# Performance work log

Measured on AMD Instinct MI355X. Metric: run time of the kernel, lower is better.

## Reference

```python
import jax, jax.numpy as jnp
import numpy as np

N = 50000      # nodes
E = 800000     # edges (before self loops)
IN_D = 128
HID = 128
OUT_D = 64
HEADS = 4
FH = HID // HEADS  # per-head feature dim
NEG_SLOPE = 0.2


def setup_inputs() -> dict:
    key = jax.random.key(0)
    ks = jax.random.split(key, 16)
    s = 0.05
    inp = {
        "x": jax.random.normal(ks[0], (N, IN_D), dtype=jnp.float32),
        "edge_index": jax.random.randint(ks[1], (2, E), 0, N, dtype=jnp.int32),
        "Wi": jax.random.normal(ks[2], (IN_D, HID), dtype=jnp.float32) * s,
        "bi": jnp.zeros((HID,), dtype=jnp.float32),
        "W0": jax.random.normal(ks[3], (HID, HID), dtype=jnp.float32) * s,
        "as0": jax.random.normal(ks[4], (HEADS, FH), dtype=jnp.float32) * s,
        "ad0": jax.random.normal(ks[5], (HEADS, FH), dtype=jnp.float32) * s,
        "b0": jnp.zeros((HID,), dtype=jnp.float32),
        "W1": jax.random.normal(ks[6], (HID, HID), dtype=jnp.float32) * s,
        "as1": jax.random.normal(ks[7], (HEADS, FH), dtype=jnp.float32) * s,
        "ad1": jax.random.normal(ks[8], (HEADS, FH), dtype=jnp.float32) * s,
        "b1": jnp.zeros((HID,), dtype=jnp.float32),
        "Wo": jax.random.normal(ks[9], (HID, OUT_D), dtype=jnp.float32) * s,
        "bo": jnp.zeros((OUT_D,), dtype=jnp.float32),
    }
    return inp


def _gat_layer(h, src, dst, W, a_src, a_dst, b):
    # h: [N, HID]; src/dst: [E'] (with self loops)
    hp = (h @ W).reshape(N, HEADS, FH)               # projected per-head features
    al_s = jnp.einsum('nhf,hf->nh', hp, a_src)       # [N, H]
    al_d = jnp.einsum('nhf,hf->nh', hp, a_dst)
    e = jax.nn.leaky_relu(al_s[src] + al_d[dst], NEG_SLOPE)  # [E', H]
    # neighbor softmax over incoming edges of each dst node (stable)
    m = jax.ops.segment_max(e, dst, num_segments=N)
    m = jnp.where(jnp.isfinite(m), m, 0.0)
    num = jnp.exp(e - m[dst])
    den = jax.ops.segment_sum(num, dst, num_segments=N)
    coef = num / (den[dst] + 1e-16)                  # [E', H]
    out = jax.ops.segment_sum(coef[:, :, None] * hp[src], dst, num_segments=N)
    return out.reshape(N, HID) + b


def reference(x, edge_index, Wi, bi, W0, as0, ad0, b0, W1, as1, ad1, b1, Wo, bo):
    # add self loops (PyG GATConv default)
    loop = jnp.arange(N, dtype=edge_index.dtype)
    src = jnp.concatenate([edge_index[0], loop])
    dst = jnp.concatenate([edge_index[1], loop])

    h = jax.nn.relu(x @ Wi + bi)
    # layer 0 (dropout = identity in eval)
    h = h + jax.nn.relu(_gat_layer(h, src, dst, W0, as0, ad0, b0))
    # layer 1
    h = h + jax.nn.relu(_gat_layer(h, src, dst, W1, as1, ad1, b1))
    return h @ Wo + bo
```

## Files before the change

### kernel.cpp

```cpp
#include <hip/hip_runtime.h>
#include <hip/hip_bf16.h>


__device__ __forceinline__ float lrelu(float x){ return x > 0.f ? x : 0.2f * x; }

typedef __attribute__((ext_vector_type(8))) short bf16x8;
typedef __attribute__((ext_vector_type(4))) float f32x4;

__device__ __forceinline__ ushort f2bf(float f){
    union { __hip_bfloat16 b; ushort u; } cv;
    cv.b = __float2bfloat16(f);
    return cv.u;
}
__device__ __forceinline__ float bf2f(short u){
    union { uint i; float f; } c;
    c.i = ((uint)(ushort)u) << 16;
    return c.f;
}

constexpr int CAP = 64;
constexpr int BUCKET_CAP = 8192;
constexpr int P1_EDGES = 2048;

__global__ __launch_bounds__(256) void bin_edges_kernel(
    const int* __restrict__ ei, int* __restrict__ gcur, int2* __restrict__ binned, int E, int N)
{
    __shared__ int hist[256], offs[256], gpos[256];
    __shared__ int2 stag[P1_EDGES];
    __shared__ int wsum[4];
    int tid = threadIdx.x;
    hist[tid] = 0;
    __syncthreads();

    int base = blockIdx.x * P1_EDGES;
    int srcv[8], dstv[8], rk[8];
    #pragma unroll
    for (int j = 0; j < 8; j++){
        int e = base + j * 256 + tid;
        if (e < E + N){
            int s, d;
            if (e < E){ s = ei[e]; d = ei[E + e]; } else { s = e - E; d = s; }
            srcv[j] = s; dstv[j] = d;
            rk[j] = atomicAdd(&hist[d >> 8], 1);
        } else dstv[j] = -1;
    }
    __syncthreads();

    int lane = tid & 63, wid = tid >> 6;
    int v = hist[tid];
    int x = v;
    #pragma unroll
    for (int o = 1; o < 64; o <<= 1){ int t = __shfl_up(x, o); if (lane >= o) x += t; }
    if (lane == 63) wsum[wid] = x;
    __syncthreads();
    int woff = 0;
    for (int w2 = 0; w2 < wid; w2++) woff += wsum[w2];
    offs[tid] = woff + x - v;
    __syncthreads();

    #pragma unroll
    for (int j = 0; j < 8; j++){
        if (dstv[j] >= 0){
            int b = dstv[j] >> 8;
            stag[offs[b] + rk[j]] = make_int2(srcv[j], dstv[j]);
        }
    }
    if (hist[tid] > 0) gpos[tid] = atomicAdd(&gcur[tid], hist[tid]);
    __syncthreads();

    int nE = offs[255] + hist[255];
    for (int i = tid; i < nE; i += 256){
        int2 p = stag[i];
        int b = p.y >> 8;
        int idx = gpos[b] + (i - offs[b]);
        if (idx < BUCKET_CAP) binned[(size_t)b * BUCKET_CAP + idx] = p;
    }
}

__global__ __launch_bounds__(256) void build_slots_kernel(
    const int* __restrict__ gcur, const int2* __restrict__ binned,
    int* __restrict__ cnt, int* __restrict__ slots, int N)
{
    __shared__ int cnt_l[256];
    __shared__ int slots_l[256][CAP];
    int tid = threadIdx.x;
    int b = blockIdx.x;
    cnt_l[tid] = 0;
    __syncthreads();

    int ne = gcur[b]; if (ne > BUCKET_CAP) ne = BUCKET_CAP;
    const int2* bp = binned + (size_t)b * BUCKET_CAP;
    for (int i = tid; i < ne; i += 256){
        int2 p = bp[i];
        int ld = p.y & 255;
        int pos = atomicAdd(&cnt_l[ld], 1);
        if (pos < CAP) slots_l[ld][pos] = p.x;
    }
    __syncthreads();

    int node = b * 256 + tid;
    if (node < N) cnt[node] = min(cnt_l[tid], CAP);
    for (int j = tid; j < 256 * CAP; j += 256){
        int n2 = b * 256 + (j >> 6);
        if (n2 < N) slots[(size_t)n2 * CAP + (j & 63)] = slots_l[j >> 6][j & 63];
    }
}

__global__ void wcast_all_kernel(const float* __restrict__ Wi, const float* __restrict__ W0,
                                 const float* __restrict__ W1, const float* __restrict__ Wo,
                                 ushort* __restrict__ ti, ushort* __restrict__ t0,
                                 ushort* __restrict__ t1, ushort* __restrict__ to_){
    int i = blockIdx.x * 256 + threadIdx.x;
    if (i < 16384){
        int k = i >> 7, n = i & 127;        ti[n * 128 + k] = f2bf(Wi[i]);
    } else if (i < 32768){
        int j = i - 16384; int k = j >> 7, n = j & 127;  t0[n * 128 + k] = f2bf(W0[j]);
    } else if (i < 49152){
        int j = i - 32768; int k = j >> 7, n = j & 127;  t1[n * 128 + k] = f2bf(W1[j]);
    } else if (i < 57344){
        int j = i - 49152; int k = j / 64, n = j % 64;   to_[n * 128 + k] = f2bf(Wo[j]);
    }
}

template<int NCOL, bool RELU, bool BIAS, bool BF16OUT, bool LOGITS, bool ABF16>
__global__ __launch_bounds__(256) void mfma_matmul_kernel(
    const void* __restrict__ Av,
    const ushort* __restrict__ Wt,
    const float* __restrict__ bias,
    void* __restrict__ Cv,
    const float* __restrict__ as_, const float* __restrict__ ad_,
    float* __restrict__ als, float* __restrict__ ald, int M)
{
    constexpr int NT = NCOL / 16;
    __shared__ ushort Ws[NCOL][136];
    int tid = threadIdx.x;
    for (int i = tid * 8; i < NCOL * 128; i += 256 * 8){
        int r = i >> 7, c = i & 127;
        *(uint4*)&Ws[r][c] = *(const uint4*)&Wt[i];
    }
    __syncthreads();

    int lane = tid & 63, wave = tid >> 6;
    int r15 = lane & 15;
    int ko  = (lane >> 4) * 8;
    int row  = blockIdx.x * 64 + wave * 16 + r15;
    int rowc = row < M ? row : M - 1;

    f32x4 acc[NT];
    #pragma unroll
    for (int t = 0; t < NT; t++) acc[t] = (f32x4){0.f, 0.f, 0.f, 0.f};

    #pragma unroll
    for (int kt = 0; kt < 4; ++kt){
        bf16x8 af;
        if (ABF16){
            af = *(const bf16x8*)&((const ushort*)Av)[(size_t)rowc * 128 + kt * 32 + ko];
        } else {
            const float* Arow = (const float*)Av + (size_t)rowc * 128;
            float4 a0 = *(const float4*)&Arow[kt * 32 + ko];
            float4 a1 = *(const float4*)&Arow[kt * 32 + ko + 4];
            af[0] = f2bf(a0.x); af[1] = f2bf(a0.y); af[2] = f2bf(a0.z); af[3] = f2bf(a0.w);
            af[4] = f2bf(a1.x); af[5] = f2bf(a1.y); af[6] = f2bf(a1.z); af[7] = f2bf(a1.w);
        }
        #pragma unroll
        for (int t = 0; t < NT; t++){
            bf16x8 bf = *(const bf16x8*)&Ws[t * 16 + r15][kt * 32 + ko];
            acc[t] = __builtin_amdgcn_mfma_f32_16x16x32_bf16(af, bf, acc[t], 0, 0, 0);
        }
    }

    int oc    = lane & 15;
    int orow0 = blockIdx.x * 64 + wave * 16 + (lane >> 4) * 4;
    #pragma unroll
    for (int t = 0; t < NT; t++){
        int ocol = t * 16 + oc;
        float bv = BIAS ? bias[ocol] : 0.f;
        #pragma unroll
        for (int rg = 0; rg < 4; rg++){
            int orow = orow0 + rg;
            if (orow < M){
                float v = acc[t][rg] + bv;
                if (RELU) v = fmaxf(v, 0.f);
                if (BF16OUT) ((ushort*)Cv)[(size_t)orow * NCOL + ocol] = f2bf(v);
                else         ((float*)Cv) [(size_t)orow * NCOL + ocol] = v;
            }
        }
    }

    if (LOGITS){
        float sva[4][4], svd[4][4];
        #pragma unroll
        for (int hh = 0; hh < 4; hh++){
            float as0v = as_[hh*32 + oc],      ad0v = ad_[hh*32 + oc];
            float as1v = as_[hh*32 + 16 + oc], ad1v = ad_[hh*32 + 16 + oc];
            #pragma unroll
            for (int rg = 0; rg < 4; rg++){
                sva[hh][rg] = acc[2*hh][rg] * as0v + acc[2*hh+1][rg] * as1v;
                svd[hh][rg] = acc[2*hh][rg] * ad0v + acc[2*hh+1][rg] * ad1v;
            }
        }
        #pragma unroll
        for (int o = 1; o < 16; o <<= 1){
            #pragma unroll
            for (int hh = 0; hh < 4; hh++)
                #pragma unroll
                for (int rg = 0; rg < 4; rg++){
                    sva[hh][rg] += __shfl_xor(sva[hh][rg], o);
                    svd[hh][rg] += __shfl_xor(svd[hh][rg], o);
                }
        }
        if (oc < 4){
            #pragma unroll
            for (int rg = 0; rg < 4; rg++){
                int orow = orow0 + rg;
                if (orow < M){
                    float va = (oc & 2) ? ((oc & 1) ? sva[3][rg] : sva[2][rg])
                                        : ((oc & 1) ? sva[1][rg] : sva[0][rg]);
                    float vd = (oc & 2) ? ((oc & 1) ? svd[3][rg] : svd[2][rg])
                                        : ((oc & 1) ? svd[1][rg] : svd[0][rg]);
                    als[orow * 4 + oc] = va;
                    ald[orow * 4 + oc] = vd;
                }
            }
        }
    }
}

__global__ __launch_bounds__(256) void gat_aggregate_kernel(
    const int* __restrict__ cnt, const int* __restrict__ slots,
    const ushort* __restrict__ hp, const float* __restrict__ als,
    const float* __restrict__ ald, const float* __restrict__ bias,
    ushort* __restrict__ h, int n)
{
    __shared__ float num_s[4][CAP * 5];
    __shared__ int   src_s[4][CAP];
    int wid = threadIdx.x >> 6;
    int lane = threadIdx.x & 63;
    int node = blockIdx.x * 4 + wid;
    float* nums = num_s[wid];
    int*   srcs = src_s[wid];

    int er = lane >> 4;
    int fg = (lane & 15) * 8;
    int head = (lane & 15) >> 2;
    int f2 = fg + er * 2;

    int deg = 0;
    float4 aldv = make_float4(0.f,0.f,0.f,0.f);
    float hold0 = 0.f, hold1 = 0.f;
    float bv0 = 0.f, bv1 = 0.f;
    if (node < n){
        deg = cnt[node];
        if (deg > CAP) deg = CAP;
        aldv = *(const float4*)&ald[node * 4];
        ushort2 h16 = *(const ushort2*)&h[(size_t)node * 128 + f2];
        hold0 = bf2f(h16.x); hold1 = bf2f(h16.y);
        bv0 = bias[f2]; bv1 = bias[f2 + 1];
    }

    float d0=0.f,d1=0.f,d2=0.f,d3=0.f;
    if (lane < deg){
        int s = slots[node * CAP + lane];
        srcs[lane] = s;
        float4 av = *(const float4*)&als[s * 4];
        d0 = __expf(lrelu(av.x + aldv.x));
        d1 = __expf(lrelu(av.y + aldv.y));
        d2 = __expf(lrelu(av.z + aldv.z));
        d3 = __expf(lrelu(av.w + aldv.w));
    }
    float s0=d0, s1=d1, s2=d2, s3=d3;
    #pragma unroll
    for (int o = 1; o < 64; o <<= 1){
        s0+=__shfl_xor(s0,o); s1+=__shfl_xor(s1,o);
        s2+=__shfl_xor(s2,o); s3+=__shfl_xor(s3,o);
    }
    float inv0=1.f/(s0+1e-16f), inv1=1.f/(s1+1e-16f);
    float inv2=1.f/(s2+1e-16f), inv3=1.f/(s3+1e-16f);
    if (lane < deg){
        nums[lane*5+0]=d0*inv0; nums[lane*5+1]=d1*inv1;
        nums[lane*5+2]=d2*inv2; nums[lane*5+3]=d3*inv3;
    }

    float a0=0.f,a1=0.f,a2=0.f,a3=0.f,a4=0.f,a5=0.f,a6=0.f,a7=0.f;
    for (int i = 0; i < deg; i += 8){
        int e0 = i + er, e1 = i + 4 + er;
        bool v0 = e0 < deg, v1 = e1 < deg;
        int ec0 = v0 ? e0 : 0, ec1 = v1 ? e1 : 0;
        int sA = srcs[ec0], sB = srcs[ec1];
        float c0 = nums[ec0*5 + head]; c0 = v0 ? c0 : 0.f;
        float c1 = nums[ec1*5 + head]; c1 = v1 ? c1 : 0.f;
        bf16x8 h0 = *(const bf16x8*)&hp[(size_t)sA * 128 + fg];
        bf16x8 h1 = *(const bf16x8*)&hp[(size_t)sB * 128 + fg];
        a0 = fmaf(c0, bf2f(h0[0]), a0); a1 = fmaf(c0, bf2f(h0[1]), a1);
        a2 = fmaf(c0, bf2f(h0[2]), a2); a3 = fmaf(c0, bf2f(h0[3]), a3);
        a4 = fmaf(c0, bf2f(h0[4]), a4); a5 = fmaf(c0, bf2f(h0[5]), a5);
        a6 = fmaf(c0, bf2f(h0[6]), a6); a7 = fmaf(c0, bf2f(h0[7]), a7);
        a0 = fmaf(c1, bf2f(h1[0]), a0); a1 = fmaf(c1, bf2f(h1[1]), a1);
        a2 = fmaf(c1, bf2f(h1[2]), a2); a3 = fmaf(c1, bf2f(h1[3]), a3);
        a4 = fmaf(c1, bf2f(h1[4]), a4); a5 = fmaf(c1, bf2f(h1[5]), a5);
        a6 = fmaf(c1, bf2f(h1[6]), a6); a7 = fmaf(c1, bf2f(h1[7]), a7);
    }
    a0 += __shfl_xor(a0,16); a0 += __shfl_xor(a0,32);
    a1 += __shfl_xor(a1,16); a1 += __shfl_xor(a1,32);
    a2 += __shfl_xor(a2,16); a2 += __shfl_xor(a2,32);
    a3 += __shfl_xor(a3,16); a3 += __shfl_xor(a3,32);
    a4 += __shfl_xor(a4,16); a4 += __shfl_xor(a4,32);
    a5 += __shfl_xor(a5,16); a5 += __shfl_xor(a5,32);
    a6 += __shfl_xor(a6,16); a6 += __shfl_xor(a6,32);
    a7 += __shfl_xor(a7,16); a7 += __shfl_xor(a7,32);

    if (node < n){
        float sA = (er & 2) ? ((er & 1) ? a6 : a4) : ((er & 1) ? a2 : a0);
        float sB = (er & 2) ? ((er & 1) ? a7 : a5) : ((er & 1) ? a3 : a1);
        float r0 = hold0 + fmaxf(sA + bv0, 0.f);
        float r1 = hold1 + fmaxf(sB + bv1, 0.f);
        ushort2 o2; o2.x = f2bf(r0); o2.y = f2bf(r1);
        *(ushort2*)&h[(size_t)node * 128 + f2] = o2;
    }
}

extern "C" void kernel_launch(void* const* d_in, const int* in_sizes, int n_in,
                              void* d_out, int out_size, void* d_ws, size_t ws_size,
                              hipStream_t stream)
{
    const float* x   = (const float*)d_in[0];
    const int*   ei  = (const int*)d_in[1];
    const float* Wi  = (const float*)d_in[2];
    const float* bi  = (const float*)d_in[3];
    const float* W0  = (const float*)d_in[4];
    const float* as0 = (const float*)d_in[5];
    const float* ad0 = (const float*)d_in[6];
    const float* b0  = (const float*)d_in[7];
    const float* W1  = (const float*)d_in[8];
    const float* as1 = (const float*)d_in[9];
    const float* ad1 = (const float*)d_in[10];
    const float* b1  = (const float*)d_in[11];
    const float* Wo  = (const float*)d_in[12];
    const float* bo  = (const float*)d_in[13];
    float* out = (float*)d_out;

    int N = in_sizes[0] / 128;
    int E = in_sizes[1] / 2;
    int EN = E + N;
    int NB = (N + 255) >> 8;

    char* w = (char*)d_ws;
    ushort* h     = (ushort*)w; w += (size_t)N * 128 * 2;
    ushort* hpb   = (ushort*)w; w += (size_t)N * 128 * 2;
    float*  als   = (float*)w;  w += (size_t)N * 4 * 4;
    float*  ald   = (float*)w;  w += (size_t)N * 4 * 4;
    int*    cnt   = (int*)w;    w += (size_t)N * 4;
    w = (char*)(((uintptr_t)w + 255) & ~(uintptr_t)255);
    int*    slots = (int*)w;    w += (size_t)N * CAP * 4;
    w = (char*)(((uintptr_t)w + 255) & ~(uintptr_t)255);
    int*    gcur  = (int*)w;    w += 256 * 4;
    w = (char*)(((uintptr_t)w + 255) & ~(uintptr_t)255);
    int2*   binned= (int2*)w;   w += (size_t)NB * BUCKET_CAP * 8;
    w = (char*)(((uintptr_t)w + 255) & ~(uintptr_t)255);
    ushort* wt_i  = (ushort*)w; w += (size_t)128 * 128 * 2;
    ushort* wt_0  = (ushort*)w; w += (size_t)128 * 128 * 2;
    ushort* wt_1  = (ushort*)w; w += (size_t)128 * 128 * 2;
    ushort* wt_o  = (ushort*)w; w += (size_t)64  * 128 * 2;

    hipMemsetAsync(gcur, 0, 256 * 4, stream);
    bin_edges_kernel<<<(EN + P1_EDGES - 1) / P1_EDGES, 256, 0, stream>>>(ei, gcur, binned, E, N);
    build_slots_kernel<<<NB, 256, 0, stream>>>(gcur, binned, cnt, slots, N);

    wcast_all_kernel<<<224, 256, 0, stream>>>(Wi, W0, W1, Wo, wt_i, wt_0, wt_1, wt_o);

    int mgrid = (N + 63) / 64;
    int agrid = (N + 3) / 4;

    mfma_matmul_kernel<128, true, true, true, false, false><<<mgrid, 256, 0, stream>>>(
        x, wt_i, bi, h, nullptr, nullptr, nullptr, nullptr, N);

    mfma_matmul_kernel<128, false, false, true, true, true><<<mgrid, 256, 0, stream>>>(
        h, wt_0, nullptr, hpb, as0, ad0, als, ald, N);
    gat_aggregate_kernel<<<agrid, 256, 0, stream>>>(cnt, slots, hpb, als, ald, b0, h, N);

    mfma_matmul_kernel<128, false, false, true, true, true><<<mgrid, 256, 0, stream>>>(
        h, wt_1, nullptr, hpb, as1, ad1, als, ald, N);
    gat_aggregate_kernel<<<agrid, 256, 0, stream>>>(cnt, slots, hpb, als, ald, b1, h, N);

    mfma_matmul_kernel<64, false, true, false, false, true><<<mgrid, 256, 0, stream>>>(
        h, wt_o, bo, out, nullptr, nullptr, nullptr, nullptr, N);
}
```

Measured before the change: 163.2 us.

## Store projected features as fp16 and aggregate with packed half2 FMAs

The projection matmul now writes hp as fp16 instead of bf16, and the aggregation kernel keeps its coefficients and accumulators in packed __half2 FMAs, which halves the ALU work in the gather loop. The matmul kernels move to 512-thread blocks of 128 rows each, which amortises the per-block weight staging into LDS. The hipMemsetAsync that zeroed gcur is dropped and the reset is folded into the weight-cast kernel. Accumulating in fp16 costs accuracy and risks range problems, and the bigger blocks may reduce occupancy.

```diff
diff --git a/kernel.cpp b/kernel.cpp
--- a/kernel.cpp
+++ b/kernel.cpp
@@ -1,5 +1,6 @@
 #include <hip/hip_runtime.h>
 #include <hip/hip_bf16.h>
+#include <hip/hip_fp16.h>
 
 
 __device__ __forceinline__ float lrelu(float x){ return x > 0.f ? x : 0.2f * x; }
@@ -109,8 +110,10 @@
 __global__ void wcast_all_kernel(const float* __restrict__ Wi, const float* __restrict__ W0,
                                  const float* __restrict__ W1, const float* __restrict__ Wo,
                                  ushort* __restrict__ ti, ushort* __restrict__ t0,
-                                 ushort* __restrict__ t1, ushort* __restrict__ to_){
+                                 ushort* __restrict__ t1, ushort* __restrict__ to_,
+                                 int* __restrict__ gcur){
     int i = blockIdx.x * 256 + threadIdx.x;
+    if (blockIdx.x == 0) gcur[threadIdx.x] = 0;
     if (i < 16384){
         int k = i >> 7, n = i & 127;        ti[n * 128 + k] = f2bf(Wi[i]);
     } else if (i < 32768){
@@ -122,8 +125,49 @@
     }
 }
 
-template<int NCOL, bool RELU, bool BIAS, bool BF16OUT, bool LOGITS, bool ABF16>
-__global__ __launch_bounds__(256) void mfma_matmul_kernel(
+__device__ __forceinline__ void epi_logits(
+    const f32x4* acc, const float* as_, const float* ad_,
+    float* als, float* ald, int oc, int orow0, int M)
+{
+    float sva[4][4], svd[4][4];
+    #pragma unroll
+    for (int hh = 0; hh < 4; hh++){
+        float as0v = as_[hh*32 + oc],      ad0v = ad_[hh*32 + oc];
+        float as1v = as_[hh*32 + 16 + oc], ad1v = ad_[hh*32 + 16 + oc];
+        #pragma unroll
+        for (int rg = 0; rg < 4; rg++){
+            sva[hh][rg] = acc[2*hh][rg] * as0v + acc[2*hh+1][rg] * as1v;
+            svd[hh][rg] = acc[2*hh][rg] * ad0v + acc[2*hh+1][rg] * ad1v;
+        }
+    }
+    #pragma unroll
+    for (int o = 1; o < 16; o <<= 1){
+        #pragma unroll
+        for (int hh = 0; hh < 4; hh++)
+            #pragma unroll
+            for (int rg = 0; rg < 4; rg++){
+                sva[hh][rg] += __shfl_xor(sva[hh][rg], o);
+                svd[hh][rg] += __shfl_xor(svd[hh][rg], o);
+            }
+    }
+    if (oc < 4){
+        #pragma unroll
+        for (int rg = 0; rg < 4; rg++){
+            int orow = orow0 + rg;
+            if (orow < M){
+                float va = (oc & 2) ? ((oc & 1) ? sva[3][rg] : sva[2][rg])
+                                    : ((oc & 1) ? sva[1][rg] : sva[0][rg]);
+                float vd = (oc & 2) ? ((oc & 1) ? svd[3][rg] : svd[2][rg])
+                                    : ((oc & 1) ? svd[1][rg] : svd[0][rg]);
+                als[orow * 4 + oc] = va;
+                ald[orow * 4 + oc] = vd;
+            }
+        }
+    }
+}
+
+template<int NCOL, bool RELU, bool BIAS, int OUTMODE, bool LOGITS, bool ABF16>
+__global__ __launch_bounds__(512) void mfma_matmul_kernel(
     const void* __restrict__ Av,
     const ushort* __restrict__ Wt,
     const float* __restrict__ bias,
@@ -134,7 +178,7 @@
     constexpr int NT = NCOL / 16;
     __shared__ ushort Ws[NCOL][136];
     int tid = threadIdx.x;
-    for (int i = tid * 8; i < NCOL * 128; i += 256 * 8){
+    for (int i = tid * 8; i < NCOL * 128; i += 512 * 8){
         int r = i >> 7, c = i & 127;
         *(uint4*)&Ws[r][c] = *(const uint4*)&Wt[i];
     }
@@ -143,7 +187,7 @@
     int lane = tid & 63, wave = tid >> 6;
     int r15 = lane & 15;
     int ko  = (lane >> 4) * 8;
-    int row  = blockIdx.x * 64 + wave * 16 + r15;
+    int row  = blockIdx.x * 128 + wave * 16 + r15;
     int rowc = row < M ? row : M - 1;
 
     f32x4 acc[NT];
@@ -170,7 +214,8 @@
     }
 
     int oc    = lane & 15;
-    int orow0 = blockIdx.x * 64 + wave * 16 + (lane >> 4) * 4;
+    int orow0 = blockIdx.x * 128 + wave * 16 + (lane >> 4) * 4;
+
     #pragma unroll
     for (int t = 0; t < NT; t++){
         int ocol = t * 16 + oc;
@@ -181,49 +226,14 @@
             if (orow < M){
                 float v = acc[t][rg] + bv;
                 if (RELU) v = fmaxf(v, 0.f);
-                if (BF16OUT) ((ushort*)Cv)[(size_t)orow * NCOL + ocol] = f2bf(v);
-                else         ((float*)Cv) [(size_t)orow * NCOL + ocol] = v;
+                if (OUTMODE == 1)      ((ushort*)Cv)[(size_t)orow * NCOL + ocol] = f2bf(v);
+                else if (OUTMODE == 3) ((ushort*)Cv)[(size_t)orow * NCOL + ocol] =
+                                           __half_as_ushort(__float2half(v));
+                else                   ((float*)Cv) [(size_t)orow * NCOL + ocol] = v;
             }
         }
     }
-
-    if (LOGITS){
-        float sva[4][4], svd[4][4];
-        #pragma unroll
-        for (int hh = 0; hh < 4; hh++){
-            float as0v = as_[hh*32 + oc],      ad0v = ad_[hh*32 + oc];
-            float as1v = as_[hh*32 + 16 + oc], ad1v = ad_[hh*32 + 16 + oc];
-            #pragma unroll
-            for (int rg = 0; rg < 4; rg++){
-                sva[hh][rg] = acc[2*hh][rg] * as0v + acc[2*hh+1][rg] * as1v;
-                svd[hh][rg] = acc[2*hh][rg] * ad0v + acc[2*hh+1][rg] * ad1v;
-            }
-        }
-        #pragma unroll
-        for (int o = 1; o < 16; o <<= 1){
-            #pragma unroll
-            for (int hh = 0; hh < 4; hh++)
-                #pragma unroll
-                for (int rg = 0; rg < 4; rg++){
-                    sva[hh][rg] += __shfl_xor(sva[hh][rg], o);
-                    svd[hh][rg] += __shfl_xor(svd[hh][rg], o);
-                }
-        }
-        if (oc < 4){
-            #pragma unroll
-            for (int rg = 0; rg < 4; rg++){
-                int orow = orow0 + rg;
-                if (orow < M){
-                    float va = (oc & 2) ? ((oc & 1) ? sva[3][rg] : sva[2][rg])
-                                        : ((oc & 1) ? sva[1][rg] : sva[0][rg]);
-                    float vd = (oc & 2) ? ((oc & 1) ? svd[3][rg] : svd[2][rg])
-                                        : ((oc & 1) ? svd[1][rg] : svd[0][rg]);
-                    als[orow * 4 + oc] = va;
-                    ald[orow * 4 + oc] = vd;
-                }
-            }
-        }
-    }
+    if (LOGITS) epi_logits(acc, as_, ad_, als, ald, oc, orow0, M);
 }
 
 __global__ __launch_bounds__(256) void gat_aggregate_kernel(
@@ -232,13 +242,13 @@
     const float* __restrict__ ald, const float* __restrict__ bias,
     ushort* __restrict__ h, int n)
 {
-    __shared__ float num_s[4][CAP * 5];
-    __shared__ int   src_s[4][CAP];
+    __shared__ uint num_s[4][CAP * 5];
+    __shared__ int  src_s[4][CAP];
     int wid = threadIdx.x >> 6;
     int lane = threadIdx.x & 63;
     int node = blockIdx.x * 4 + wid;
-    float* nums = num_s[wid];
-    int*   srcs = src_s[wid];
+    uint* nums = num_s[wid];
+    int*  srcs = src_s[wid];
 
     int er = lane >> 4;
     int fg = (lane & 15) * 8;
@@ -277,29 +287,45 @@
     float inv0=1.f/(s0+1e-16f), inv1=1.f/(s1+1e-16f);
     float inv2=1.f/(s2+1e-16f), inv3=1.f/(s3+1e-16f);
     if (lane < deg){
-        nums[lane*5+0]=d0*inv0; nums[lane*5+1]=d1*inv1;
-        nums[lane*5+2]=d2*inv2; nums[lane*5+3]=d3*inv3;
-    }
-
-    float a0=0.f,a1=0.f,a2=0.f,a3=0.f,a4=0.f,a5=0.f,a6=0.f,a7=0.f;
+        __half2 c0 = __half2half2(__float2half(d0*inv0));
+        __half2 c1 = __half2half2(__float2half(d1*inv1));
+        __half2 c2 = __half2half2(__float2half(d2*inv2));
+        __half2 c3 = __half2half2(__float2half(d3*inv3));
+        nums[lane*5+0] = *(uint*)&c0;
+        nums[lane*5+1] = *(uint*)&c1;
+        nums[lane*5+2] = *(uint*)&c2;
+        nums[lane*5+3] = *(uint*)&c3;
+    }
+
+    __half2 A0 = __half2half2(__float2half(0.f));
+    __half2 A1 = A0, A2 = A0, A3 = A0;
     for (int i = 0; i < deg; i += 8){
         int e0 = i + er, e1 = i + 4 + er;
         bool v0 = e0 < deg, v1 = e1 < deg;
         int ec0 = v0 ? e0 : 0, ec1 = v1 ? e1 : 0;
         int sA = srcs[ec0], sB = srcs[ec1];
-        float c0 = nums[ec0*5 + head]; c0 = v0 ? c0 : 0.f;
-        float c1 = nums[ec1*5 + head]; c1 = v1 ? c1 : 0.f;
-        bf16x8 h0 = *(const bf16x8*)&hp[(size_t)sA * 128 + fg];
-        bf16x8 h1 = *(const bf16x8*)&hp[(size_t)sB * 128 + fg];
-        a0 = fmaf(c0, bf2f(h0[0]), a0); a1 = fmaf(c0, bf2f(h0[1]), a1);
-        a2 = fmaf(c0, bf2f(h0[2]), a2); a3 = fmaf(c0, bf2f(h0[3]), a3);
-        a4 = fmaf(c0, bf2f(h0[4]), a4); a5 = fmaf(c0, bf2f(h0[5]), a5);
-        a6 = fmaf(c0, bf2f(h0[6]), a6); a7 = fmaf(c0, bf2f(h0[7]), a7);
-        a0 = fmaf(c1, bf2f(h1[0]), a0); a1 = fmaf(c1, bf2f(h1[1]), a1);
-        a2 = fmaf(c1, bf2f(h1[2]), a2); a3 = fmaf(c1, bf2f(h1[3]), a3);
-        a4 = fmaf(c1, bf2f(h1[4]), a4); a5 = fmaf(c1, bf2f(h1[5]), a5);
-        a6 = fmaf(c1, bf2f(h1[6]), a6); a7 = fmaf(c1, bf2f(h1[7]), a7);
-    }
+        uint cu0 = nums[ec0*5 + head]; cu0 = v0 ? cu0 : 0u;
+        uint cu1 = nums[ec1*5 + head]; cu1 = v1 ? cu1 : 0u;
+        __half2 c20 = *(__half2*)&cu0;
+        __half2 c21 = *(__half2*)&cu1;
+        uint4 hv0 = *(const uint4*)&hp[(size_t)sA * 128 + fg];
+        uint4 hv1 = *(const uint4*)&hp[(size_t)sB * 128 + fg];
+        A0 = __hfma2(c20, *(__half2*)&hv0.x, A0);
+        A1 = __hfma2(c20, *(__half2*)&hv0.y, A1);
+        A2 = __hfma2(c20, *(__half2*)&hv0.z, A2);
+        A3 = __hfma2(c20, *(__half2*)&hv0.w, A3);
+        A0 = __hfma2(c21, *(__half2*)&hv1.x, A0);
+        A1 = __hfma2(c21, *(__half2*)&hv1.y, A1);
+        A2 = __hfma2(c21, *(__half2*)&hv1.z, A2);
+        A3 = __hfma2(c21, *(__half2*)&hv1.w, A3);
+    }
+    float2 f01 = __half22float2(A0);
+    float2 f23 = __half22float2(A1);
+    float2 f45 = __half22float2(A2);
+    float2 f67 = __half22float2(A3);
+    float a0=f01.x, a1=f01.y, a2=f23.x, a3=f23.y;
+    float a4=f45.x, a5=f45.y, a6=f67.x, a7=f67.y;
+
     a0 += __shfl_xor(a0,16); a0 += __shfl_xor(a0,32);
     a1 += __shfl_xor(a1,16); a1 += __shfl_xor(a1,32);
     a2 += __shfl_xor(a2,16); a2 += __shfl_xor(a2,32);
@@ -345,43 +371,42 @@
     int NB = (N + 255) >> 8;
 
     char* w = (char*)d_ws;
-    ushort* h     = (ushort*)w; w += (size_t)N * 128 * 2;
-    ushort* hpb   = (ushort*)w; w += (size_t)N * 128 * 2;
-    float*  als   = (float*)w;  w += (size_t)N * 4 * 4;
-    float*  ald   = (float*)w;  w += (size_t)N * 4 * 4;
-    int*    cnt   = (int*)w;    w += (size_t)N * 4;
+    ushort* h     = (ushort*)w;      w += (size_t)N * 128 * 2;
+    ushort* hpq   = (ushort*)w;      w += (size_t)N * 128 * 2;
+    float*  als   = (float*)w;       w += (size_t)N * 4 * 4;
+    float*  ald   = (float*)w;       w += (size_t)N * 4 * 4;
+    int*    cnt   = (int*)w;         w += (size_t)N * 4;
     w = (char*)(((uintptr_t)w + 255) & ~(uintptr_t)255);
-    int*    slots = (int*)w;    w += (size_t)N * CAP * 4;
+    int*    slots = (int*)w;         w += (size_t)N * CAP * 4;
     w = (char*)(((uintptr_t)w + 255) & ~(uintptr_t)255);
-    int*    gcur  = (int*)w;    w += 256 * 4;
+    int*    gcur  = (int*)w;         w += 256 * 4;
     w = (char*)(((uintptr_t)w + 255) & ~(uintptr_t)255);
-    int2*   binned= (int2*)w;   w += (size_t)NB * BUCKET_CAP * 8;
+    int2*   binned= (int2*)w;        w += (size_t)NB * BUCKET_CAP * 8;
     w = (char*)(((uintptr_t)w + 255) & ~(uintptr_t)255);
-    ushort* wt_i  = (ushort*)w; w += (size_t)128 * 128 * 2;
-    ushort* wt_0  = (ushort*)w; w += (size_t)128 * 128 * 2;
-    ushort* wt_1  = (ushort*)w; w += (size_t)128 * 128 * 2;
-    ushort* wt_o  = (ushort*)w; w += (size_t)64  * 128 * 2;
-
-    hipMemsetAsync(gcur, 0, 256 * 4, stream);
+    ushort* wt_i  = (ushort*)w;      w += (size_t)128 * 128 * 2;
+    ushort* wt_0  = (ushort*)w;      w += (size_t)128 * 128 * 2;
+    ushort* wt_1  = (ushort*)w;      w += (size_t)128 * 128 * 2;
+    ushort* wt_o  = (ushort*)w;      w += (size_t)64  * 128 * 2;
+
+    int mgrid = (N + 127) / 128;
+    int agrid = (N + 3) / 4;
+
+    wcast_all_kernel<<<224, 256, 0, stream>>>(Wi, W0, W1, Wo, wt_i, wt_0, wt_1, wt_o, gcur);
+
     bin_edges_kernel<<<(EN + P1_EDGES - 1) / P1_EDGES, 256, 0, stream>>>(ei, gcur, binned, E, N);
     build_slots_kernel<<<NB, 256, 0, stream>>>(gcur, binned, cnt, slots, N);
 
-    wcast_all_kernel<<<224, 256, 0, stream>>>(Wi, W0, W1, Wo, wt_i, wt_0, wt_1, wt_o);
-
-    int mgrid = (N + 63) / 64;
-    int agrid = (N + 3) / 4;
-
-    mfma_matmul_kernel<128, true, true, true, false, false><<<mgrid, 256, 0, stream>>>(
+    mfma_matmul_kernel<128, true, true, 1, false, false><<<mgrid, 512, 0, stream>>>(
         x, wt_i, bi, h, nullptr, nullptr, nullptr, nullptr, N);
 
-    mfma_matmul_kernel<128, false, false, true, true, true><<<mgrid, 256, 0, stream>>>(
-        h, wt_0, nullptr, hpb, as0, ad0, als, ald, N);
-    gat_aggregate_kernel<<<agrid, 256, 0, stream>>>(cnt, slots, hpb, als, ald, b0, h, N);
-
-    mfma_matmul_kernel<128, false, false, true, true, true><<<mgrid, 256, 0, stream>>>(
-        h, wt_1, nullptr, hpb, as1, ad1, als, ald, N);
-    gat_aggregate_kernel<<<agrid, 256, 0, stream>>>(cnt, slots, hpb, als, ald, b1, h, N);
-
-    mfma_matmul_kernel<64, false, true, false, false, true><<<mgrid, 256, 0, stream>>>(
+    mfma_matmul_kernel<128, false, false, 3, true, true><<<mgrid, 512, 0, stream>>>(
+        h, wt_0, nullptr, hpq, as0, ad0, als, ald, N);
+    gat_aggregate_kernel<<<agrid, 256, 0, stream>>>(cnt, slots, hpq, als, ald, b0, h, N);
+
+    mfma_matmul_kernel<128, false, false, 3, true, true><<<mgrid, 512, 0, stream>>>(
+        h, wt_1, nullptr, hpq, as1, ad1, als, ald, N);
+    gat_aggregate_kernel<<<agrid, 256, 0, stream>>>(cnt, slots, hpq, als, ald, b1, h, N);
+
+    mfma_matmul_kernel<64, false, true, 0, false, true><<<mgrid, 512, 0, stream>>>(
         h, wt_o, bo, out, nullptr, nullptr, nullptr, nullptr, N);
 }
```

Result: no change. 161.0 us (-1.3%).
